# Kernel tuning notes

Measured on AMD Instinct MI355X. Metric: run time of the kernel, lower is better.

The kernel has to match this reference:

```python
import jax, jax.numpy as jnp
import numpy as np

N, P, S, ENT = 256, 4, 40, 60
E = 1 + P + S + ENT          # 105 graph nodes (query + paras + sents + ents)
D = 1024                     # input_dim == hidden_dim
H, T = 8, 3                  # gnn heads, edge types
DH = D // H                  # per-head output dim
NEG = -1e30


def setup_inputs() -> dict:
    key = jax.random.key(0)
    ks = jax.random.split(key, 12)
    f = lambda k, sh, s: jax.random.normal(k, sh, jnp.float32) * s
    return {
        "query_vec": f(ks[0], (N, D), 1.0),
        "para_state": f(ks[1], (N, P, D), 1.0),
        "sent_state": f(ks[2], (N, S, D), 1.0),
        "ent_state": f(ks[3], (N, ENT, D), 1.0),
        "para_mask": jax.random.randint(ks[4], (N, P), 0, 2).astype(jnp.float32),
        "sent_mask": jax.random.randint(ks[5], (N, S), 0, 2).astype(jnp.float32),
        "ent_mask": jax.random.randint(ks[6], (N, ENT), 0, 2).astype(jnp.float32),
        "adj": jax.random.randint(ks[7], (N, E, E), 0, T + 1).astype(jnp.int32),
        "W": f(ks[8], (H, T, D, DH), 0.05),        # per head/edge-type projection
        "a": f(ks[9], (H, T, 2 * DH), 0.05),       # GAT attention vector [a1;a2]
        "qW1": f(ks[10], (H, T, D, 2 * DH), 0.05), # query-gate layer 1
        "qW2": f(ks[11], (H, T, 2 * DH, 2 * DH), 0.05),  # query-gate layer 2
    }


def _graph_block(x, query_vec, node_mask, adj, W, a, qW1, qW2):
    # x: [N,E,D], node_mask: [N,E,1], adj: [N,E,E] int (0 = no edge, 1..T = edge type)
    # per head/edge-type projections: [H,T,N,E,DH]
    h = jnp.einsum('ned,htdk->htnek', x, W)
    # query-conditioned gate (q_attn=True): sigmoid(relu(q @ W1) @ W2) -> [H,T,N,2DH]
    g = jax.nn.sigmoid(jnp.einsum('htnk,htkm->htnm',
                                  jax.nn.relu(jnp.einsum('nd,htdk->htnk', query_vec, qW1)),
                                  qW2))
    # decomposed GAT score: score[i,j] = lrelu((g1*h_i)@a1 + (g2*h_j)@a2)
    a1, a2 = a[..., :DH], a[..., DH:]
    f1 = jnp.einsum('htnek,htnk->htne', h, g[..., :DH] * a1[:, :, None, :])
    f2 = jnp.einsum('htnek,htnk->htne', h, g[..., DH:] * a2[:, :, None, :])
    score = jax.nn.leaky_relu(f1[..., :, None] + f2[..., None, :], 0.2)  # [H,T,N,E,E]
    # accumulate only where adj matches the edge type (i+1)
    etype = (jnp.arange(T, dtype=adj.dtype) + 1)[None, :, None, None, None]
    scores = jnp.sum(jnp.where(adj[None, None] == etype, score, 0.0), axis=1)  # [H,N,E,E]
    scores = jnp.where(adj[None] > 0, scores, NEG)
    coefs = jax.nn.softmax(scores, axis=-1)                 # [H,N,E,E]
    # original uses the last edge-type projection, node-masked, for aggregation
    h_last = h[:, -1] * node_mask[None]                     # [H,N,E,DH]
    out = jnp.einsum('hnij,hnjd->hnid', coefs, h_last)      # [H,N,E,DH]
    out = jnp.transpose(out, (1, 2, 0, 3)).reshape(x.shape[0], E, H * DH)
    out = jax.nn.relu(out)                                  # dropout p=0 in eval
    return out + x                                          # residual (identity align)


def reference(query_vec, para_state, sent_state, ent_state,
              para_mask, sent_mask, ent_mask, adj, W, a, qW1, qW2):
    x = jnp.concatenate([query_vec[:, None, :], para_state, sent_state, ent_state], axis=1)  # [N,E,D]
    node_mask = jnp.concatenate(
        [jnp.ones((x.shape[0], 1), x.dtype), para_mask, sent_mask, ent_mask], axis=-1)[..., None]  # [N,E,1]
    graph_state = _graph_block(x, query_vec, node_mask, adj, W, a, qW1, qW2)  # [N,E,D]
    return graph_state
```

## Files before the change

kernel.cpp:

```cpp
#include <hip/hip_runtime.h>
#include <stdint.h>


typedef unsigned short u16;
typedef __bf16 bf16;
typedef __bf16 bf16x8 __attribute__((ext_vector_type(8)));
typedef float f32x4 __attribute__((ext_vector_type(4)));

#define N_ 256
#define E_ 105
#define D_ 1024
#define H_ 8
#define DH_ 128
#define NE_ 26880

__device__ __forceinline__ u16 f2b(float f) { bf16 h = (bf16)f; return __builtin_bit_cast(u16, h); }
__device__ __forceinline__ float b2f(u16 u) { bf16 h = __builtin_bit_cast(bf16, u); return (float)h; }

#define AS1 __attribute__((address_space(1)))
#define AS3 __attribute__((address_space(3)))

__device__ __forceinline__ void load16_lds(const void* g, void* l) {
  __builtin_amdgcn_global_load_lds((AS1 void*)(unsigned long long)(uintptr_t)g,
                                   (AS3 void*)l, 16, 0, 0);
}

__device__ __forceinline__ void gemm128(const u16* A, const u16* B, int K,
                                        int lda, int ldb, f32x4 (&acc)[4][4]) {
  __shared__ u16 lA[8192];
  __shared__ u16 lB[8192];
  const int tid  = threadIdx.x;
  const int lane = tid & 63;
  const int wave = tid >> 6;
  const int ln15 = lane & 15;
  const int lq   = lane >> 4;
  const int wRow = (wave >> 1) * 64;
  const int wCol = (wave & 1) * 64;

  const int iters = K >> 6;
  for (int kt = 0; kt < iters; ++kt) {
    const char* Ab = (const char*)A + kt * 128;
    const char* Bb = (const char*)B + kt * 128;
#pragma unroll
    for (int m = 0; m < 4; ++m) {
      int ci  = m * 256 + tid;
      int row = ci >> 3;
      int g   = (ci & 7) ^ (row & 7);
      char* dstA = (char*)lA + m * 4096 + wave * 1024;
      char* dstB = (char*)lB + m * 4096 + wave * 1024;
      load16_lds(Ab + (long)row * ((long)lda * 2) + g * 16, dstA);
      load16_lds(Bb + (long)row * ((long)ldb * 2) + g * 16, dstB);
    }
    __syncthreads();
#pragma unroll
    for (int ks = 0; ks < 2; ++ks) {
      const int cc = ks * 4 + lq;
      bf16x8 af[4], bfv[4];
#pragma unroll
      for (int i = 0; i < 4; ++i) {
        int r = wRow + i * 16 + ln15;
        af[i] = *(const bf16x8*)&lA[r * 64 + ((cc ^ (r & 7)) << 3)];
        int c = wCol + i * 16 + ln15;
        bfv[i] = *(const bf16x8*)&lB[c * 64 + ((cc ^ (c & 7)) << 3)];
      }
#pragma unroll
      for (int i = 0; i < 4; ++i)
#pragma unroll
        for (int j = 0; j < 4; ++j)
          acc[i][j] = __builtin_amdgcn_mfma_f32_16x16x32_bf16(af[i], bfv[j], acc[i][j], 0, 0, 0);
    }
    __syncthreads();
  }
}

__device__ __forceinline__ void zero_acc(f32x4 (&acc)[4][4]) {
  f32x4 z = {0.f, 0.f, 0.f, 0.f};
#pragma unroll
  for (int i = 0; i < 4; ++i)
#pragma unroll
    for (int j = 0; j < 4; ++j) acc[i][j] = z;
}

__global__ __launch_bounds__(256) void k_cast(const float* src, u16* dst, long n) {
  long i = ((long)blockIdx.x * 256 + threadIdx.x) * 4;
  if (i >= n) return;
  float4 v = *(const float4*)(src + i);
  ushort4 o;
  o.x = f2b(v.x); o.y = f2b(v.y); o.z = f2b(v.z); o.w = f2b(v.w);
  *(ushort4*)(dst + i) = o;
}

__global__ __launch_bounds__(256) void k_build(const float* q, const float* para,
                                               const float* sent, const float* ent,
                                               const float* pm, const float* sm,
                                               const float* em, u16* x, float* nmask) {
  long idx = (long)blockIdx.x * 256 + threadIdx.x;
  if (idx >= (long)NE_ * 128) return;
  int ne = (int)(idx >> 7), dc = (int)(idx & 127);
  int n = ne / E_, e = ne - n * E_;
  const float* src;
  if (e == 0)      src = q + (long)n * D_;
  else if (e < 5)  src = para + (long)(n * 4 + (e - 1)) * D_;
  else if (e < 45) src = sent + (long)(n * 40 + (e - 5)) * D_;
  else             src = ent + (long)(n * 60 + (e - 45)) * D_;
  float4 v0 = *(const float4*)(src + dc * 8);
  float4 v1 = *(const float4*)(src + dc * 8 + 4);
  uint4 o;
  o.x = (unsigned)f2b(v0.x) | ((unsigned)f2b(v0.y) << 16);
  o.y = (unsigned)f2b(v0.z) | ((unsigned)f2b(v0.w) << 16);
  o.z = (unsigned)f2b(v1.x) | ((unsigned)f2b(v1.y) << 16);
  o.w = (unsigned)f2b(v1.z) | ((unsigned)f2b(v1.w) << 16);
  *(uint4*)(x + (long)ne * D_ + dc * 8) = o;
  if (dc == 0) {
    float mv;
    if (e == 0)      mv = 1.f;
    else if (e < 5)  mv = pm[n * 4 + e - 1];
    else if (e < 45) mv = sm[n * 40 + e - 5];
    else             mv = em[n * 60 + e - 45];
    nmask[ne] = mv;
  }
}

__global__ __launch_bounds__(256) void k_tr(const float* src, u16* dst, int R, int C,
                                            long sStr, long dStr) {
  __shared__ u16 t[32][33];
  const int bz = blockIdx.y;
  const int tilesC = C >> 5;
  const int tr = (blockIdx.x / tilesC) << 5;
  const int tc = (blockIdx.x % tilesC) << 5;
  const int lr = threadIdx.x >> 5;
  const int lc = threadIdx.x & 31;
#pragma unroll
  for (int i = 0; i < 4; ++i)
    t[lr + i * 8][lc] = f2b(src[bz * sStr + (long)(tr + lr + i * 8) * C + tc + lc]);
  __syncthreads();
#pragma unroll
  for (int i = 0; i < 4; ++i)
    dst[bz * dStr + (long)(tc + lr + i * 8) * R + tr + lc] = t[lc][lr + i * 8];
}

__global__ __launch_bounds__(256) void k_qw1(const u16* x, const u16* qW1t, u16* r_bf) {
  const int bx = blockIdx.x;
  const int ht = bx >> 2, nt = (bx >> 1) & 1, mt = bx & 1;
  f32x4 acc[4][4];
  zero_acc(acc);
  gemm128(x + (long)nt * 128 * (E_ * D_), qW1t + ((long)ht * 256 + mt * 128) * D_,
          1024, E_ * D_, 1024, acc);
  const int tid = threadIdx.x, lane = tid & 63, wave = tid >> 6;
  const int ln15 = lane & 15, lq = lane >> 4;
  const int wRow = (wave >> 1) * 64, wCol = (wave & 1) * 64;
#pragma unroll
  for (int rt = 0; rt < 4; ++rt)
#pragma unroll
    for (int ct = 0; ct < 4; ++ct)
#pragma unroll
      for (int rg = 0; rg < 4; ++rg) {
        int n = nt * 128 + wRow + rt * 16 + lq * 4 + rg;
        int m = mt * 128 + wCol + ct * 16 + ln15;
        float v = acc[rt][ct][rg];
        if (v < 0.f) v = 0.f;
        r_bf[((long)ht * 256 + n) * 256 + m] = f2b(v);
      }
}

__global__ __launch_bounds__(256) void k_qw2(const u16* r_bf, const u16* qW2t, const float* a,
                                             u16* ga) {
  const int bx = blockIdx.x;
  const int ht = bx >> 2, nt = (bx >> 1) & 1, mt = bx & 1;
  f32x4 acc[4][4];
  zero_acc(acc);
  gemm128(r_bf + ((long)ht * 256 + nt * 128) * 256, qW2t + ((long)ht * 256 + mt * 128) * 256,
          256, 256, 256, acc);
  const int tid = threadIdx.x, lane = tid & 63, wave = tid >> 6;
  const int ln15 = lane & 15, lq = lane >> 4;
  const int wRow = (wave >> 1) * 64, wCol = (wave & 1) * 64;
#pragma unroll
  for (int rt = 0; rt < 4; ++rt)
#pragma unroll
    for (int ct = 0; ct < 4; ++ct)
#pragma unroll
      for (int rg = 0; rg < 4; ++rg) {
        int n = nt * 128 + wRow + rt * 16 + lq * 4 + rg;
        int m = mt * 128 + wCol + ct * 16 + ln15;
        float v = acc[rt][ct][rg];
        float sig = 1.f / (1.f + __expf(-v));
        float gv = sig * a[ht * 256 + m];
        int s = m >> 7, kk = m & 127;
        ga[(((long)ht * 2 + s) * 256 + n) * 128 + kk] = f2b(gv);
      }
}

__global__ __launch_bounds__(256) void k_w12(const u16* ga, const u16* Wb, u16* w12) {
  const int bx = blockIdx.x;
  const int c = bx >> 4, r2 = bx & 15;
  const int nt = r2 >> 3, dt = r2 & 7;
  const int ht = c >> 1;
  f32x4 acc[4][4];
  zero_acc(acc);
  gemm128(ga + ((long)c * 256 + nt * 128) * 128, Wb + (long)ht * 131072 + dt * 128 * 128,
          128, 128, 128, acc);
  const int tid = threadIdx.x, lane = tid & 63, wave = tid >> 6;
  const int ln15 = lane & 15, lq = lane >> 4;
  const int wRow = (wave >> 1) * 64, wCol = (wave & 1) * 64;
#pragma unroll
  for (int rt = 0; rt < 4; ++rt)
#pragma unroll
    for (int ct = 0; ct < 4; ++ct)
#pragma unroll
      for (int rg = 0; rg < 4; ++rg) {
        int n = nt * 128 + wRow + rt * 16 + lq * 4 + rg;
        int d = dt * 128 + wCol + ct * 16 + ln15;
        w12[((long)n * 48 + c) * 1024 + d] = f2b(acc[rt][ct][rg]);
      }
}

__global__ __launch_bounds__(256) void k_f(const u16* x, const u16* w12, float* F) {
  const int n = blockIdx.x;
  f32x4 acc[4][4];
  zero_acc(acc);
  gemm128(x + (long)n * E_ * D_, w12 + (long)n * 48 * 1024, 1024, 1024, 1024, acc);
  const int tid = threadIdx.x, lane = tid & 63, wave = tid >> 6;
  const int ln15 = lane & 15, lq = lane >> 4;
  const int wRow = (wave >> 1) * 64, wCol = (wave & 1) * 64;
#pragma unroll
  for (int rt = 0; rt < 4; ++rt)
#pragma unroll
    for (int ct = 0; ct < 4; ++ct)
#pragma unroll
      for (int rg = 0; rg < 4; ++rg) {
        int e = wRow + rt * 16 + lq * 4 + rg;
        int c = wCol + ct * 16 + ln15;
        if (e < 105 && c < 48) F[((long)n * 48 + c) * 105 + e] = acc[rt][ct][rg];
      }
}

__global__ __launch_bounds__(256) void k_h(const u16* x, const u16* Wt, const float* nmask,
                                           float* out) {
  const int bx = blockIdx.x;
  const int h = bx / 210;
  const int ne0 = (bx % 210) * 128;
  f32x4 acc[4][4];
  zero_acc(acc);
  gemm128(x + (long)ne0 * D_, Wt + (long)h * DH_ * D_, 1024, 1024, 1024, acc);
  const int tid = threadIdx.x, lane = tid & 63, wave = tid >> 6;
  const int ln15 = lane & 15, lq = lane >> 4;
  const int wRow = (wave >> 1) * 64, wCol = (wave & 1) * 64;
#pragma unroll
  for (int rt = 0; rt < 4; ++rt)
#pragma unroll
    for (int ct = 0; ct < 4; ++ct)
#pragma unroll
      for (int rg = 0; rg < 4; ++rg) {
        int ne = ne0 + wRow + rt * 16 + lq * 4 + rg;
        int k = wCol + ct * 16 + ln15;
        float mv = nmask[ne];
        out[(long)ne * D_ + h * DH_ + k] = acc[rt][ct][rg] * mv;
      }
}

__global__ __launch_bounds__(256) void k_attn(const float* F, const int* adj, const u16* x,
                                              float* out) {
  const int h = blockIdx.x >> 8;
  const int n = blockIdx.x & 255;
  __shared__ u16 cb[112 * 128];
  __shared__ u16 hT[128 * 128];
  __shared__ float f1s[3][112];
  __shared__ float f2s[3][112];
  const int tid = threadIdx.x;
  const int lane = tid & 63, wave = tid >> 6;

  for (int i = tid; i < 630; i += 256) {
    int t = i / 210;
    int rm = i - t * 210;
    int s = rm / 105;
    int e = rm - s * 105;
    float v = F[((long)n * 48 + (h * 3 + t) * 2 + s) * 105 + e];
    if (s == 0) f1s[t][e] = v; else f2s[t][e] = v;
  }
  {
    unsigned* cbz = (unsigned*)cb;
    for (int i = tid; i < 112 * 64; i += 256) cbz[i] = 0;
  }
  for (int i = tid; i < 105 * 32; i += 256) {
    int j = i >> 5, kc = i & 31;
    float4 v = *(const float4*)(out + ((long)(n * 105 + j)) * D_ + h * DH_ + kc * 4);
    int jc = j >> 3, jl = j & 7;
    int k0 = kc * 4;
    hT[(k0 + 0) * 128 + ((jc ^ ((k0 + 0) & 15)) << 3) + jl] = f2b(v.x);
    hT[(k0 + 1) * 128 + ((jc ^ ((k0 + 1) & 15)) << 3) + jl] = f2b(v.y);
    hT[(k0 + 2) * 128 + ((jc ^ ((k0 + 2) & 15)) << 3) + jl] = f2b(v.z);
    hT[(k0 + 3) * 128 + ((jc ^ ((k0 + 3) & 15)) << 3) + jl] = f2b(v.w);
  }
  for (int i = tid; i < 128 * 23; i += 256) {
    int k = i / 23;
    int j = 105 + (i - k * 23);
    int jc = j >> 3, jl = j & 7;
    hT[k * 128 + ((jc ^ (k & 15)) << 3) + jl] = 0;
  }
  __syncthreads();

  {
    const int j1 = 64 + lane;
    float f20a = f2s[0][lane], f20b = f2s[1][lane], f20c = f2s[2][lane];
    float f21a = 0.f, f21b = 0.f, f21c = 0.f;
    if (lane < 41) { f21a = f2s[0][j1]; f21b = f2s[1][j1]; f21c = f2s[2][j1]; }
    for (int i = wave; i < 105; i += 4) {
      const int* arow = adj + (long)n * (E_ * E_) + i * E_;
      int av0 = arow[lane];
      int av1 = (lane < 41) ? arow[j1] : 0;
      float f11 = f1s[0][i], f12 = f1s[1][i], f13 = f1s[2][i];
      float s0, s1;
      {
        float f1v = (av0 == 1) ? f11 : ((av0 == 2) ? f12 : f13);
        float f2v = (av0 == 1) ? f20a : ((av0 == 2) ? f20b : f20c);
        float s = f1v + f2v;
        s = (s < 0.f) ? 0.2f * s : s;
        s0 = (av0 > 0) ? s : -1e30f;
      }
      {
        float f1v = (av1 == 1) ? f11 : ((av1 == 2) ? f12 : f13);
        float f2v = (av1 == 1) ? f21a : ((av1 == 2) ? f21b : f21c);
        float s = f1v + f2v;
        s = (s < 0.f) ? 0.2f * s : s;
        s1 = (av1 > 0) ? s : -1e30f;
      }
      float m = fmaxf(s0, s1);
#pragma unroll
      for (int d = 1; d < 64; d <<= 1) m = fmaxf(m, __shfl_xor(m, d));
      float e0 = __expf(s0 - m);
      float e1 = (lane < 41) ? __expf(s1 - m) : 0.f;
      float sum = e0 + e1;
#pragma unroll
      for (int d = 1; d < 64; d <<= 1) sum += __shfl_xor(sum, d);
      float inv = 1.f / sum;
      const int rsw = i & 15;
      cb[i * 128 + ((((lane >> 3) ^ rsw) << 3) + (lane & 7))] = f2b(e0 * inv);
      if (lane < 41)
        cb[i * 128 + ((((j1 >> 3) ^ rsw) << 3) + (lane & 7))] = f2b(e1 * inv);
    }
  }
  __syncthreads();

  const int ln15 = lane & 15, lq = lane >> 4;
  const int nmt = (wave < 3) ? 2 : 1;
  f32x4 acc[2][8];
  {
    f32x4 z = {0.f, 0.f, 0.f, 0.f};
#pragma unroll
    for (int a_ = 0; a_ < 2; ++a_)
#pragma unroll
      for (int b_ = 0; b_ < 8; ++b_) acc[a_][b_] = z;
  }
#pragma unroll
  for (int ks = 0; ks < 4; ++ks) {
    const int cc = ks * 4 + lq;
    bf16x8 bfr[8];
#pragma unroll
    for (int jn = 0; jn < 8; ++jn) {
      int k = jn * 16 + ln15;
      bfr[jn] = *(const bf16x8*)&hT[k * 128 + ((cc ^ (k & 15)) << 3)];
    }
#pragma unroll
    for (int im = 0; im < 2; ++im) {
      if (im < nmt) {
        int i = (wave + im * 4) * 16 + ln15;
        bf16x8 af = *(const bf16x8*)&cb[i * 128 + ((cc ^ (i & 15)) << 3)];
#pragma unroll
        for (int jn = 0; jn < 8; ++jn)
          acc[im][jn] = __builtin_amdgcn_mfma_f32_16x16x32_bf16(af, bfr[jn], acc[im][jn], 0, 0, 0);
      }
    }
  }
  for (int im = 0; im < nmt; ++im)
    for (int jn = 0; jn < 8; ++jn)
#pragma unroll
      for (int rg = 0; rg < 4; ++rg) {
        int i = (wave + im * 4) * 16 + lq * 4 + rg;
        if (i < 105) {
          int k = jn * 16 + ln15;
          long off = ((long)(n * E_ + i)) * D_ + h * DH_ + k;
          float v = acc[im][jn][rg];
          v = v < 0.f ? 0.f : v;
          out[off] = v + b2f(x[off]);
        }
      }
}

extern "C" void kernel_launch(void* const* d_in, const int* in_sizes, int n_in,
                              void* d_out, int out_size, void* d_ws, size_t ws_size,
                              hipStream_t stream) {
  const float* q    = (const float*)d_in[0];
  const float* para = (const float*)d_in[1];
  const float* sent = (const float*)d_in[2];
  const float* ent  = (const float*)d_in[3];
  const float* pm   = (const float*)d_in[4];
  const float* sm   = (const float*)d_in[5];
  const float* em   = (const float*)d_in[6];
  const int*   adj  = (const int*)d_in[7];
  const float* W    = (const float*)d_in[8];
  const float* a    = (const float*)d_in[9];
  const float* qW1  = (const float*)d_in[10];
  const float* qW2  = (const float*)d_in[11];
  float* out = (float*)d_out;
  char* ws = (char*)d_ws;

  u16*   x     = (u16*)(ws);
  float* nmask = (float*)(ws + 55050240);
  u16*   Wb    = (u16*)(ws + 55682048);
  u16*   Wt    = (u16*)(ws + 61973504);
  u16*   qW1t  = (u16*)(ws + 64070656);
  u16*   qW2t  = (u16*)(ws + 76653568);
  u16*   r_bf  = (u16*)(ws + 79799296);
  u16*   ga    = (u16*)(ws + 82945024);
  u16*   w12   = (u16*)(ws + 86090752);
  float* F     = (float*)(ws + 111420416);

  k_build<<<13440, 256, 0, stream>>>(q, para, sent, ent, pm, sm, em, x, nmask);
  k_cast<<<3072, 256, 0, stream>>>(W, Wb, 3145728);
  k_tr<<<dim3(256, 24), 256, 0, stream>>>(qW1, qW1t, 1024, 256, 262144, 262144);
  k_tr<<<dim3(64, 24), 256, 0, stream>>>(qW2, qW2t, 256, 256, 65536, 65536);
  k_tr<<<dim3(128, 8), 256, 0, stream>>>(W + 262144, Wt, 1024, 128, 393216, 131072);
  k_qw1<<<96, 256, 0, stream>>>(x, qW1t, r_bf);
  k_qw2<<<96, 256, 0, stream>>>(r_bf, qW2t, a, ga);
  k_w12<<<768, 256, 0, stream>>>(ga, Wb, w12);
  k_f<<<256, 256, 0, stream>>>(x, w12, F);
  k_h<<<1680, 256, 0, stream>>>(x, Wt, nmask, out);
  k_attn<<<2048, 256, 0, stream>>>(F, adj, x, out);
}
```

Baseline: 704.2 us.

## Store h projection transposed in bf16 and load MFMA B-fragments from global

k_h now stages its tile in shared memory and writes the masked projection as bf16 in a transposed per-(n,h) layout packed inside the output buffer, zero-padding columns past 104. k_attn drops the hT shared-memory transpose and loads the B operand fragments straight from global memory. It also prefetches the next adjacency row in the softmax loop. Shared memory is now passed explicitly to gemm128. This cuts fp32 write and read traffic and the LDS transpose, at the cost of an aliased in-place workspace in the output that must be read before it is overwritten, which the added barrier is meant to ensure.

```diff
diff --git a/kernel.cpp b/kernel.cpp
--- a/kernel.cpp
+++ b/kernel.cpp
@@ -25,10 +25,10 @@
                                    (AS3 void*)l, 16, 0, 0);
 }
 
-__device__ __forceinline__ void gemm128(const u16* A, const u16* B, int K,
+__device__ __forceinline__ void gemm128(u16* lds, const u16* A, const u16* B, int K,
                                         int lda, int ldb, f32x4 (&acc)[4][4]) {
-  __shared__ u16 lA[8192];
-  __shared__ u16 lB[8192];
+  u16* lA = lds;
+  u16* lB = lds + 8192;
   const int tid  = threadIdx.x;
   const int lane = tid & 63;
   const int wave = tid >> 6;
@@ -140,11 +140,12 @@
 }
 
 __global__ __launch_bounds__(256) void k_qw1(const u16* x, const u16* qW1t, u16* r_bf) {
+  __shared__ u16 shm[16384];
   const int bx = blockIdx.x;
   const int ht = bx >> 2, nt = (bx >> 1) & 1, mt = bx & 1;
   f32x4 acc[4][4];
   zero_acc(acc);
-  gemm128(x + (long)nt * 128 * (E_ * D_), qW1t + ((long)ht * 256 + mt * 128) * D_,
+  gemm128(shm, x + (long)nt * 128 * (E_ * D_), qW1t + ((long)ht * 256 + mt * 128) * D_,
           1024, E_ * D_, 1024, acc);
   const int tid = threadIdx.x, lane = tid & 63, wave = tid >> 6;
   const int ln15 = lane & 15, lq = lane >> 4;
@@ -165,11 +166,12 @@
 
 __global__ __launch_bounds__(256) void k_qw2(const u16* r_bf, const u16* qW2t, const float* a,
                                              u16* ga) {
+  __shared__ u16 shm[16384];
   const int bx = blockIdx.x;
   const int ht = bx >> 2, nt = (bx >> 1) & 1, mt = bx & 1;
   f32x4 acc[4][4];
   zero_acc(acc);
-  gemm128(r_bf + ((long)ht * 256 + nt * 128) * 256, qW2t + ((long)ht * 256 + mt * 128) * 256,
+  gemm128(shm, r_bf + ((long)ht * 256 + nt * 128) * 256, qW2t + ((long)ht * 256 + mt * 128) * 256,
           256, 256, 256, acc);
   const int tid = threadIdx.x, lane = tid & 63, wave = tid >> 6;
   const int ln15 = lane & 15, lq = lane >> 4;
@@ -191,13 +193,14 @@
 }
 
 __global__ __launch_bounds__(256) void k_w12(const u16* ga, const u16* Wb, u16* w12) {
+  __shared__ u16 shm[16384];
   const int bx = blockIdx.x;
   const int c = bx >> 4, r2 = bx & 15;
   const int nt = r2 >> 3, dt = r2 & 7;
   const int ht = c >> 1;
   f32x4 acc[4][4];
   zero_acc(acc);
-  gemm128(ga + ((long)c * 256 + nt * 128) * 128, Wb + (long)ht * 131072 + dt * 128 * 128,
+  gemm128(shm, ga + ((long)c * 256 + nt * 128) * 128, Wb + (long)ht * 131072 + dt * 128 * 128,
           128, 128, 128, acc);
   const int tid = threadIdx.x, lane = tid & 63, wave = tid >> 6;
   const int ln15 = lane & 15, lq = lane >> 4;
@@ -215,10 +218,11 @@
 }
 
 __global__ __launch_bounds__(256) void k_f(const u16* x, const u16* w12, float* F) {
+  __shared__ u16 shm[16384];
   const int n = blockIdx.x;
   f32x4 acc[4][4];
   zero_acc(acc);
-  gemm128(x + (long)n * E_ * D_, w12 + (long)n * 48 * 1024, 1024, 1024, 1024, acc);
+  gemm128(shm, x + (long)n * E_ * D_, w12 + (long)n * 48 * 1024, 1024, 1024, 1024, acc);
   const int tid = threadIdx.x, lane = tid & 63, wave = tid >> 6;
   const int ln15 = lane & 15, lq = lane >> 4;
   const int wRow = (wave >> 1) * 64, wCol = (wave & 1) * 64;
@@ -236,12 +240,13 @@
 
 __global__ __launch_bounds__(256) void k_h(const u16* x, const u16* Wt, const float* nmask,
                                            float* out) {
+  __shared__ u16 shm[16384];
   const int bx = blockIdx.x;
   const int h = bx / 210;
   const int ne0 = (bx % 210) * 128;
   f32x4 acc[4][4];
   zero_acc(acc);
-  gemm128(x + (long)ne0 * D_, Wt + (long)h * DH_ * D_, 1024, 1024, 1024, acc);
+  gemm128(shm, x + (long)ne0 * D_, Wt + (long)h * DH_ * D_, 1024, 1024, 1024, acc);
   const int tid = threadIdx.x, lane = tid & 63, wave = tid >> 6;
   const int ln15 = lane & 15, lq = lane >> 4;
   const int wRow = (wave >> 1) * 64, wCol = (wave & 1) * 64;
@@ -251,11 +256,31 @@
     for (int ct = 0; ct < 4; ++ct)
 #pragma unroll
       for (int rg = 0; rg < 4; ++rg) {
-        int ne = ne0 + wRow + rt * 16 + lq * 4 + rg;
-        int k = wCol + ct * 16 + ln15;
-        float mv = nmask[ne];
-        out[(long)ne * D_ + h * DH_ + k] = acc[rt][ct][rg] * mv;
-      }
+        int nel = wRow + rt * 16 + lq * 4 + rg;
+        int k   = wCol + ct * 16 + ln15;
+        shm[k * 128 + (nel ^ ((k & 15) << 3))] = f2b(acc[rt][ct][rg]);
+      }
+  __syncthreads();
+  char* ob = (char*)out;
+  for (int it = tid; it < 16384; it += 256) {
+    int k = it >> 7, nel = it & 127;
+    int ne = ne0 + nel;
+    int n = ne / 105;
+    int j = ne - n * 105;
+    int t = k * 224 + j * 2;
+    long gb = ((long)(n * 105 + (t >> 9)) << 12) + ((long)h << 9) + (t & 511);
+    u16 v = shm[k * 128 + (nel ^ ((k & 15) << 3))];
+    float mv = nmask[ne];
+    *(u16*)(ob + gb) = (mv != 0.f) ? v : (u16)0;
+    if (j == 104) {
+#pragma unroll
+      for (int p = 1; p <= 7; ++p) {
+        int tp = t + p * 2;
+        long gp = ((long)(n * 105 + (tp >> 9)) << 12) + ((long)h << 9) + (tp & 511);
+        *(u16*)(ob + gp) = 0;
+      }
+    }
+  }
 }
 
 __global__ __launch_bounds__(256) void k_attn(const float* F, const int* adj, const u16* x,
@@ -263,7 +288,6 @@
   const int h = blockIdx.x >> 8;
   const int n = blockIdx.x & 255;
   __shared__ u16 cb[112 * 128];
-  __shared__ u16 hT[128 * 128];
   __shared__ float f1s[3][112];
   __shared__ float f2s[3][112];
   const int tid = threadIdx.x;
@@ -281,33 +305,25 @@
     unsigned* cbz = (unsigned*)cb;
     for (int i = tid; i < 112 * 64; i += 256) cbz[i] = 0;
   }
-  for (int i = tid; i < 105 * 32; i += 256) {
-    int j = i >> 5, kc = i & 31;
-    float4 v = *(const float4*)(out + ((long)(n * 105 + j)) * D_ + h * DH_ + kc * 4);
-    int jc = j >> 3, jl = j & 7;
-    int k0 = kc * 4;
-    hT[(k0 + 0) * 128 + ((jc ^ ((k0 + 0) & 15)) << 3) + jl] = f2b(v.x);
-    hT[(k0 + 1) * 128 + ((jc ^ ((k0 + 1) & 15)) << 3) + jl] = f2b(v.y);
-    hT[(k0 + 2) * 128 + ((jc ^ ((k0 + 2) & 15)) << 3) + jl] = f2b(v.z);
-    hT[(k0 + 3) * 128 + ((jc ^ ((k0 + 3) & 15)) << 3) + jl] = f2b(v.w);
-  }
-  for (int i = tid; i < 128 * 23; i += 256) {
-    int k = i / 23;
-    int j = 105 + (i - k * 23);
-    int jc = j >> 3, jl = j & 7;
-    hT[k * 128 + ((jc ^ (k & 15)) << 3) + jl] = 0;
-  }
   __syncthreads();
 
   {
+    const int* abase = adj + (long)n * (E_ * E_);
     const int j1 = 64 + lane;
+    const bool j1v = lane < 41;
     float f20a = f2s[0][lane], f20b = f2s[1][lane], f20c = f2s[2][lane];
     float f21a = 0.f, f21b = 0.f, f21c = 0.f;
-    if (lane < 41) { f21a = f2s[0][j1]; f21b = f2s[1][j1]; f21c = f2s[2][j1]; }
-    for (int i = wave; i < 105; i += 4) {
-      const int* arow = adj + (long)n * (E_ * E_) + i * E_;
-      int av0 = arow[lane];
-      int av1 = (lane < 41) ? arow[j1] : 0;
+    if (j1v) { f21a = f2s[0][j1]; f21b = f2s[1][j1]; f21c = f2s[2][j1]; }
+    int i = wave;
+    int av0 = abase[i * E_ + lane];
+    int av1 = j1v ? abase[i * E_ + j1] : 0;
+    while (i < 105) {
+      const int inext = i + 4;
+      int bv0 = 0, bv1 = 0;
+      if (inext < 105) {
+        bv0 = abase[inext * E_ + lane];
+        bv1 = j1v ? abase[inext * E_ + j1] : 0;
+      }
       float f11 = f1s[0][i], f12 = f1s[1][i], f13 = f1s[2][i];
       float s0, s1;
       {
@@ -328,19 +344,22 @@
 #pragma unroll
       for (int d = 1; d < 64; d <<= 1) m = fmaxf(m, __shfl_xor(m, d));
       float e0 = __expf(s0 - m);
-      float e1 = (lane < 41) ? __expf(s1 - m) : 0.f;
+      float e1 = j1v ? __expf(s1 - m) : 0.f;
       float sum = e0 + e1;
 #pragma unroll
       for (int d = 1; d < 64; d <<= 1) sum += __shfl_xor(sum, d);
       float inv = 1.f / sum;
       const int rsw = i & 15;
       cb[i * 128 + ((((lane >> 3) ^ rsw) << 3) + (lane & 7))] = f2b(e0 * inv);
-      if (lane < 41)
+      if (j1v)
         cb[i * 128 + ((((j1 >> 3) ^ rsw) << 3) + (lane & 7))] = f2b(e1 * inv);
+      av0 = bv0; av1 = bv1;
+      i = inext;
     }
   }
   __syncthreads();
 
+  const char* hb = (const char*)out + (((long)n * 105) << 12) + ((long)h << 9);
   const int ln15 = lane & 15, lq = lane >> 4;
   const int nmt = (wave < 3) ? 2 : 1;
   f32x4 acc[2][8];
@@ -354,11 +373,13 @@
 #pragma unroll
   for (int ks = 0; ks < 4; ++ks) {
     const int cc = ks * 4 + lq;
+    const int ccb = (cc < 14) ? cc : 0;
     bf16x8 bfr[8];
 #pragma unroll
     for (int jn = 0; jn < 8; ++jn) {
       int k = jn * 16 + ln15;
-      bfr[jn] = *(const bf16x8*)&hT[k * 128 + ((cc ^ (k & 15)) << 3)];
+      int t = k * 224 + ccb * 16;
+      bfr[jn] = *(const bf16x8*)(hb + ((long)(t >> 9) << 12) + (t & 511));
     }
 #pragma unroll
     for (int im = 0; im < 2; ++im) {
@@ -371,6 +392,7 @@
       }
     }
   }
+  __syncthreads();
   for (int im = 0; im < nmt; ++im)
     for (int jn = 0; jn < 8; ++jn)
 #pragma unroll
```

Measured after the change: 707.8 us. Within noise of the previous version (+0.5%).
